# Kernel tuning notes

Measured on AMD Instinct MI355X. Metric: run time of the kernel, lower is better.

## Reference

```python
import jax, jax.numpy as jnp
import numpy as np

TAU = 1.5      # lif_tau
V_TH = 1.0     # spikingjelly default v_threshold
EPS = 1e-5     # BatchNorm eps
ALPHA = 4.0    # spikingjelly default sigmoid surrogate alpha

@jax.custom_vjp
def spike_fn(x):
    return (x >= 0.0).astype(x.dtype)

def _spike_fwd(x):
    return spike_fn(x), x

def _spike_bwd(x, g):
    s = jax.nn.sigmoid(ALPHA * x)
    return (g * ALPHA * s * (1.0 - s),)

spike_fn.defvjp(_spike_fwd, _spike_bwd)

def lif(x):
    # x: [T, B, C, N]; hard reset to 0, decay_input=True, detach_reset=True
    def step(v, xt):
        v = v + (xt - v) / TAU
        s = spike_fn(v - V_TH)
        sd = jax.lax.stop_gradient(s)
        v = (1.0 - sd) * v
        return v, s
    _, spikes = jax.lax.scan(step, jnp.zeros_like(x[0]), x)
    return spikes

def bn(x, gamma, beta, mean, var):
    # eval-mode BatchNorm1d over channel dim of [B, C, L]
    inv = gamma * jax.lax.rsqrt(var + EPS)
    return x * inv[None, :, None] + (beta - mean * inv)[None, :, None]

def setup_inputs() -> dict:
    key = jax.random.key(0)
    ks = jax.random.split(key, 13)
    B, C, T, N, H = 8, 256, 4, 4096, 1024
    return {
        "x": jax.random.normal(ks[0], (B, C, T, N), jnp.float32),
        "fc1_w": jax.random.normal(ks[1], (H, C), jnp.float32) * 0.05,
        "fc1_b": jax.random.normal(ks[2], (H,), jnp.float32) * 0.05,
        "fc2_w": jax.random.normal(ks[3], (C, H), jnp.float32) * 0.05,
        "fc2_b": jax.random.normal(ks[4], (C,), jnp.float32) * 0.05,
        "bn1_gamma": jax.random.uniform(ks[5], (H,), jnp.float32, 0.5, 1.5),
        "bn1_beta": jax.random.normal(ks[6], (H,), jnp.float32) * 0.1,
        "bn1_mean": jax.random.normal(ks[7], (H,), jnp.float32) * 0.1,
        "bn1_var": jax.random.uniform(ks[8], (H,), jnp.float32, 0.5, 1.5),
        "bn2_gamma": jax.random.uniform(ks[9], (C,), jnp.float32, 0.5, 1.5),
        "bn2_beta": jax.random.normal(ks[10], (C,), jnp.float32) * 0.1,
        "bn2_mean": jax.random.normal(ks[11], (C,), jnp.float32) * 0.1,
        "bn2_var": jax.random.uniform(ks[12], (C,), jnp.float32, 0.5, 1.5),
    }

def reference(x, fc1_w, fc1_b, fc2_w, fc2_b,
              bn1_gamma, bn1_beta, bn1_mean, bn1_var,
              bn2_gamma, bn2_beta, bn2_mean, bn2_var):
    B, C, T, N = x.shape
    H = fc1_w.shape[0]
    # fc2_bn on raw input, then LIF over T
    h = bn(x.reshape(B, C, T * N), bn2_gamma, bn2_beta, bn2_mean, bn2_var)
    h = h.reshape(B, C, T, N).transpose(2, 0, 1, 3)          # [T,B,C,N]
    h = lif(h).transpose(1, 2, 0, 3).reshape(B, C, T * N)    # [B,C,TN]
    # fc1: 1x1 conv == GEMM over channels
    h = jnp.einsum('hc,bcl->bhl', fc1_w, h) + fc1_b[None, :, None]
    h = bn(h, bn1_gamma, bn1_beta, bn1_mean, bn1_var)
    h = h.reshape(B, H, T, N).transpose(2, 0, 1, 3)          # [T,B,H,N]
    h = lif(h).transpose(1, 2, 0, 3).reshape(B, H, T * N)    # [B,H,TN]
    # fc2
    h = jnp.einsum('ch,bhl->bcl', fc2_w, h) + fc2_b[None, :, None]
    return h.reshape(B, C, T, N)
```

## Files before the change

kernel.cpp:

```cpp
#include <hip/hip_runtime.h>

#define BB 8
#define CC 256
#define TT 4
#define NNv 4096
#define HH 1024
#define LLv (TT*NNv)

typedef int int4v __attribute__((ext_vector_type(4)));

static __device__ __forceinline__ void barrier_keep_vmem() {
    asm volatile("s_waitcnt lgkmcnt(0)" ::: "memory");
    __builtin_amdgcn_s_barrier();
    __builtin_amdgcn_sched_barrier(0);
}

__global__ __launch_bounds__(256) void k_prep1(const float* __restrict__ w,
                                               unsigned char* __restrict__ wd)
{
    int i = blockIdx.x * 256 + threadIdx.x;
    int h = i >> 8, c = i & 255;
    int w24 = __float2int_rn(w[i] * 16777216.0f);
    int d2 = ((w24 + 128) & 255) - 128;  w24 = (w24 - d2) >> 8;
    int d1 = ((w24 + 128) & 255) - 128;  w24 = (w24 - d1) >> 8;
    int d0 = w24;
    size_t off = ((((size_t)(h >> 6) * 4 + (c >> 6)) * 4 + ((h >> 4) & 3)) << 10)
               + ((c >> 4) & 3) * 256 + (h & 15) * 16 + (c & 15);
    wd[off] = (unsigned char)d0;
    wd[262144 + off] = (unsigned char)d1;
    wd[2 * 262144 + off] = (unsigned char)d2;
}

__global__ __launch_bounds__(256) void k_prep2(const float* __restrict__ w,
                                               unsigned char* __restrict__ wd)
{
    int i = blockIdx.x * 256 + threadIdx.x;
    int c = i >> 10, h = i & 1023;
    int w16 = __float2int_rn(w[i] * 65536.0f);
    int d1 = ((w16 + 128) & 255) - 128;  w16 = (w16 - d1) >> 8;
    int d0 = w16;
    size_t off = ((((((size_t)(c >> 6) * 8 + (h >> 7)) * 2 + ((h >> 6) & 1)) * 4
                    + ((c >> 4) & 3)) << 10)
                 + ((h >> 4) & 3) * 256 + (c & 15) * 16 + (h & 15));
    wd[off] = (unsigned char)d0;
    wd[262144 + off] = (unsigned char)d1;
}

__global__ __launch_bounds__(256) void k_bn2_lif_t(
    const float* __restrict__ x,
    const float* __restrict__ g, const float* __restrict__ be,
    const float* __restrict__ mu, const float* __restrict__ va,
    unsigned char* __restrict__ s1T, int b0)
{
    __shared__ unsigned char ts[TT][64][80];
    int tx = threadIdx.x;
    int n0 = blockIdx.x * 64;
    int c0 = blockIdx.y * 64;
    int bl = blockIdx.z;
    int b  = b0 + bl;
    int cl = tx >> 2, np = tx & 3;
    int c = c0 + cl;
    float rsq = __fdiv_rn(1.0f, __fsqrt_rn(__fadd_rn(va[c], 1e-5f)));
    float inv = __fmul_rn(g[c], rsq);
    float add = __fsub_rn(be[c], __fmul_rn(mu[c], inv));
    size_t xb = ((size_t)(b * CC + c) * TT) * NNv + n0 + np * 16;
    float v[16];
    #pragma unroll
    for (int i = 0; i < 16; i++) v[i] = 0.0f;
    #pragma unroll
    for (int t = 0; t < TT; t++) {
        float4 p[4];
        #pragma unroll
        for (int k = 0; k < 4; k++) p[k] = *(const float4*)(x + xb + (size_t)t * NNv + 4 * k);
        const float* xp = (const float*)p;
        unsigned int ob[4] = {0, 0, 0, 0};
        #pragma unroll
        for (int i = 0; i < 16; i++) {
            float y = __fadd_rn(__fmul_rn(xp[i], inv), add);
            float vv = __fadd_rn(v[i], __fdiv_rn(__fsub_rn(y, v[i]), 1.5f));
            bool sp = vv >= 1.0f;
            v[i] = sp ? 0.0f : vv;
            if (sp) ob[i >> 2] |= 1u << (8 * (i & 3));
        }
        uint4 pk; pk.x = ob[0]; pk.y = ob[1]; pk.z = ob[2]; pk.w = ob[3];
        *(uint4*)&ts[t][cl][np * 16] = pk;
    }
    __syncthreads();
    int nl = tx >> 2, cp = tx & 3;
    #pragma unroll
    for (int t = 0; t < TT; t++) {
        unsigned int u[4];
        #pragma unroll
        for (int kk = 0; kk < 4; kk++) {
            u[kk] = (unsigned int)ts[t][cp * 16 + kk * 4 + 0][nl]
                  | ((unsigned int)ts[t][cp * 16 + kk * 4 + 1][nl] << 8)
                  | ((unsigned int)ts[t][cp * 16 + kk * 4 + 2][nl] << 16)
                  | ((unsigned int)ts[t][cp * 16 + kk * 4 + 3][nl] << 24);
        }
        uint4 pk; pk.x = u[0]; pk.y = u[1]; pk.z = u[2]; pk.w = u[3];
        *(uint4*)(s1T + ((size_t)(bl * TT + t) * NNv + n0 + nl) * CC + c0 + cp * 16) = pk;
    }
}

__global__ __launch_bounds__(256, 3) void k_gemm1_lif(
    const unsigned char* __restrict__ w1d,
    const float* __restrict__ b1,
    const float* __restrict__ g1, const float* __restrict__ be1,
    const float* __restrict__ mu1, const float* __restrict__ va1,
    const unsigned char* __restrict__ s1T, unsigned char* __restrict__ s2T)
{
    __shared__ unsigned char Ls[TT * 32][80];
    const int tx = threadIdx.x;
    const int n0 = blockIdx.x * 32;
    const int ht = blockIdx.y;
    const int bl = blockIdx.z;
    const int lane = tx & 63, w = tx >> 6;
    const int q = lane >> 4, ln = lane & 15;
    const int mh = (w & 1) * 32, wn = (w >> 1) * 16;
    const int h0 = ht * 64;

    int4v a0[TT][2], a1[TT][2], a2[TT][2];
    #pragma unroll
    for (int t = 0; t < TT; t++)
    #pragma unroll
    for (int mi = 0; mi < 2; mi++) {
        a0[t][mi] = (int4v){0, 0, 0, 0};
        a1[t][mi] = (int4v){0, 0, 0, 0};
        a2[t][mi] = (int4v){0, 0, 0, 0};
    }

    unsigned long long d[2][4];
    #pragma unroll
    for (int i = 0; i < 4; i++) {
        int task = i * 256 + tx;
        int cb = task & 7, nr = (task >> 3) & 31, t = task >> 8;
        d[0][i] = *(const unsigned long long*)(
            s1T + ((size_t)(bl * TT + t) * NNv + n0 + nr) * CC + 0 * 64 + cb * 8);
    }

    #pragma unroll
    for (int ko = 0; ko < 4; ko++) {
        const int cur = ko & 1;
        if (ko > 0) barrier_keep_vmem();
        #pragma unroll
        for (int i = 0; i < 4; i++) {
            int task = i * 256 + tx;
            int cb = task & 7, nr = (task >> 3) & 31, t = task >> 8;
            *(unsigned long long*)&Ls[t * 32 + nr][cb * 8] = d[cur][i];
        }
        if (ko < 3) {
            #pragma unroll
            for (int i = 0; i < 4; i++) {
                int task = i * 256 + tx;
                int cb = task & 7, nr = (task >> 3) & 31, t = task >> 8;
                d[cur ^ 1][i] = *(const unsigned long long*)(
                    s1T + ((size_t)(bl * TT + t) * NNv + n0 + nr) * CC + (ko + 1) * 64 + cb * 8);
            }
        }
        barrier_keep_vmem();

        int4v sf[TT];
        #pragma unroll
        for (int t = 0; t < TT; t++)
            sf[t] = *(const int4v*)&Ls[t * 32 + wn + ln][q * 16];
        int4v w0[2], w1[2], w2[2];
        #pragma unroll
        for (int mi = 0; mi < 2; mi++) {
            size_t fb = ((((size_t)ht * 4 + ko) * 4 + (mh >> 4) + mi) << 10) + lane * 16;
            w0[mi] = *(const int4v*)(w1d + fb);
            w1[mi] = *(const int4v*)(w1d + 262144 + fb);
            w2[mi] = *(const int4v*)(w1d + 2 * 262144 + fb);
        }
        #pragma unroll
        for (int t = 0; t < TT; t++)
        #pragma unroll
        for (int mi = 0; mi < 2; mi++) {
            a0[t][mi] = __builtin_amdgcn_mfma_i32_16x16x64_i8(w0[mi], sf[t], a0[t][mi], 0, 0, 0);
            a1[t][mi] = __builtin_amdgcn_mfma_i32_16x16x64_i8(w1[mi], sf[t], a1[t][mi], 0, 0, 0);
            a2[t][mi] = __builtin_amdgcn_mfma_i32_16x16x64_i8(w2[mi], sf[t], a2[t][mi], 0, 0, 0);
        }
    }

    const int l_n = n0 + wn + ln;
    #pragma unroll
    for (int mi = 0; mi < 2; mi++) {
        float invr[4], addr_[4], biasr[4];
        #pragma unroll
        for (int r = 0; r < 4; r++) {
            int h = h0 + mh + mi * 16 + q * 4 + r;
            float rsq = __fdiv_rn(1.0f, __fsqrt_rn(__fadd_rn(va1[h], 1e-5f)));
            invr[r] = __fmul_rn(g1[h], rsq);
            addr_[r] = __fsub_rn(be1[h], __fmul_rn(mu1[h], invr[r]));
            biasr[r] = b1[h];
        }
        float v4[4] = {0.f, 0.f, 0.f, 0.f};
        #pragma unroll
        for (int t = 0; t < TT; t++) {
            int4v ci = (((a0[t][mi] << 8) + a1[t][mi]) << 8) + a2[t][mi];
            unsigned int pk = 0;
            #pragma unroll
            for (int r = 0; r < 4; r++) {
                float h1 = __fadd_rn(__fmul_rn((float)ci[r], 5.9604644775390625e-08f),
                                     biasr[r]);
                float y  = __fadd_rn(__fmul_rn(h1, invr[r]), addr_[r]);
                float vv = __fadd_rn(v4[r], __fdiv_rn(__fsub_rn(y, v4[r]), 1.5f));
                bool sp = vv >= 1.0f;
                v4[r] = sp ? 0.0f : vv;
                if (sp) pk |= (1u << (8 * r));
            }
            *(unsigned int*)(s2T + ((size_t)bl * LLv + t * NNv + l_n) * HH
                             + h0 + mh + mi * 16 + q * 4) = pk;
        }
    }
}

__global__ __launch_bounds__(256, 3) void k_gemm2(
    const unsigned char* __restrict__ w2d,
    const float* __restrict__ b2c,
    const unsigned char* __restrict__ s2T, float* __restrict__ outp, int b0)
{
    __shared__ unsigned char Ls[64][144];
    const int tx = threadIdx.x;
    const int l0 = blockIdx.x * 64;
    const int ct = blockIdx.y;
    const int bl = blockIdx.z;
    const int b  = b0 + bl;
    const int lane = tx & 63, w = tx >> 6;
    const int q = lane >> 4, ln = lane & 15;
    const int mc = (w & 1) * 32, wl = (w >> 1) * 32;

    int4v a0[2][2], a1[2][2];
    #pragma unroll
    for (int mi = 0; mi < 2; mi++)
    #pragma unroll
    for (int ni = 0; ni < 2; ni++) {
        a0[mi][ni] = (int4v){0, 0, 0, 0};
        a1[mi][ni] = (int4v){0, 0, 0, 0};
    }

    unsigned long long d[2][4];
    #pragma unroll
    for (int i = 0; i < 4; i++) {
        int task = i * 256 + tx;
        int hb = task & 15, lr = task >> 4;
        d[0][i] = *(const unsigned long long*)(
            s2T + ((size_t)bl * LLv + l0 + lr) * HH + 0 * 128 + hb * 8);
    }

    #pragma unroll
    for (int ko = 0; ko < 8; ko++) {
        const int cur = ko & 1;
        if (ko > 0) barrier_keep_vmem();
        #pragma unroll
        for (int i = 0; i < 4; i++) {
            int task = i * 256 + tx;
            int hb = task & 15, lr = task >> 4;
            *(unsigned long long*)&Ls[lr][hb * 8] = d[cur][i];
        }
        if (ko < 7) {
            #pragma unroll
            for (int i = 0; i < 4; i++) {
                int task = i * 256 + tx;
                int hb = task & 15, lr = task >> 4;
                d[cur ^ 1][i] = *(const unsigned long long*)(
                    s2T + ((size_t)bl * LLv + l0 + lr) * HH + (ko + 1) * 128 + hb * 8);
            }
        }
        barrier_keep_vmem();

        #pragma unroll
        for (int kb = 0; kb < 2; kb++) {
            int4v sf[2];
            #pragma unroll
            for (int ni = 0; ni < 2; ni++)
                sf[ni] = *(const int4v*)&Ls[wl + ni * 16 + ln][kb * 64 + q * 16];
            int4v w0[2], w1[2];
            #pragma unroll
            for (int mi = 0; mi < 2; mi++) {
                size_t fb = ((((((size_t)ct * 8 + ko) * 2 + kb) * 4 + (mc >> 4) + mi)) << 10)
                          + lane * 16;
                w0[mi] = *(const int4v*)(w2d + fb);
                w1[mi] = *(const int4v*)(w2d + 262144 + fb);
            }
            #pragma unroll
            for (int mi = 0; mi < 2; mi++)
            #pragma unroll
            for (int ni = 0; ni < 2; ni++) {
                a0[mi][ni] = __builtin_amdgcn_mfma_i32_16x16x64_i8(w0[mi], sf[ni], a0[mi][ni], 0, 0, 0);
                a1[mi][ni] = __builtin_amdgcn_mfma_i32_16x16x64_i8(w1[mi], sf[ni], a1[mi][ni], 0, 0, 0);
            }
        }
    }
    #pragma unroll
    for (int mi = 0; mi < 2; mi++)
    #pragma unroll
    for (int ni = 0; ni < 2; ni++) {
        int4v tv = (a0[mi][ni] << 8) + a1[mi][ni];
        #pragma unroll
        for (int r = 0; r < 4; r++) {
            int c = ct * 64 + mc + mi * 16 + q * 4 + r;
            int l = l0 + wl + ni * 16 + ln;
            outp[((size_t)b * CC + c) * LLv + l] =
                __fadd_rn(__fmul_rn((float)tv[r], 1.52587890625e-05f), b2c[c]);
        }
    }
}

extern "C" void kernel_launch(void* const* d_in, const int* in_sizes, int n_in,
                              void* d_out, int out_size, void* d_ws, size_t ws_size,
                              hipStream_t stream) {
    const float* x    = (const float*)d_in[0];
    const float* fc1w = (const float*)d_in[1];
    const float* fc1b = (const float*)d_in[2];
    const float* fc2w = (const float*)d_in[3];
    const float* fc2b = (const float*)d_in[4];
    const float* g1   = (const float*)d_in[5];
    const float* be1  = (const float*)d_in[6];
    const float* mu1  = (const float*)d_in[7];
    const float* va1  = (const float*)d_in[8];
    const float* g2   = (const float*)d_in[9];
    const float* be2  = (const float*)d_in[10];
    const float* mu2  = (const float*)d_in[11];
    const float* va2  = (const float*)d_in[12];

    const size_t WB  = (size_t)3 * 262144 + (size_t)2 * 262144;
    const size_t S1B = (size_t)TT * NNv * CC;
    const size_t S2B = (size_t)LLv * HH;

    int nbc;
    bool full_s1;
    if      (ws_size >= WB + 8 * S1B + 8 * S2B) { nbc = 8; full_s1 = true;  }
    else if (ws_size >= WB + 8 * S1B + 4 * S2B) { nbc = 4; full_s1 = true;  }
    else if (ws_size >= WB + 8 * S1B + 2 * S2B) { nbc = 2; full_s1 = true;  }
    else if (ws_size >= WB + 8 * S1B + 1 * S2B) { nbc = 1; full_s1 = true;  }
    else                                        { nbc = 1; full_s1 = false; }

    unsigned char* w1d = (unsigned char*)d_ws;
    unsigned char* w2d = w1d + (size_t)3 * 262144;
    unsigned char* s1T = w2d + (size_t)2 * 262144;
    unsigned char* s2T = s1T + (full_s1 ? (size_t)8 * S1B : S1B);
    float* outp = (float*)d_out;

    hipLaunchKernelGGL(k_prep1, dim3(1024), dim3(256), 0, stream, fc1w, w1d);
    hipLaunchKernelGGL(k_prep2, dim3(1024), dim3(256), 0, stream, fc2w, w2d);

    if (full_s1) {
        hipLaunchKernelGGL(k_bn2_lif_t, dim3(NNv / 64, CC / 64, BB), dim3(256), 0, stream,
                           x, g2, be2, mu2, va2, s1T, 0);
        for (int b0 = 0; b0 < BB; b0 += nbc) {
            hipLaunchKernelGGL(k_gemm1_lif, dim3(NNv / 32, HH / 64, nbc), dim3(256), 0, stream,
                               w1d, fc1b, g1, be1, mu1, va1, s1T + (size_t)b0 * S1B, s2T);
            hipLaunchKernelGGL(k_gemm2, dim3(LLv / 64, CC / 64, nbc), dim3(256), 0, stream,
                               w2d, fc2b, s2T, outp, b0);
        }
    } else {
        for (int b0 = 0; b0 < BB; ++b0) {
            hipLaunchKernelGGL(k_bn2_lif_t, dim3(NNv / 64, CC / 64, 1), dim3(256), 0, stream,
                               x, g2, be2, mu2, va2, s1T, b0);
            hipLaunchKernelGGL(k_gemm1_lif, dim3(NNv / 32, HH / 64, 1), dim3(256), 0, stream,
                               w1d, fc1b, g1, be1, mu1, va1, s1T, s2T);
            hipLaunchKernelGGL(k_gemm2, dim3(LLv / 64, CC / 64, 1), dim3(256), 0, stream,
                               w2d, fc2b, s2T, outp, b0);
        }
    }
}
```

Baseline: 607.2 us.

## Stage gemm1 spike output through LDS and widen gemm2 channel tile

In the first GEMM kernel, per-lane 4-byte spike stores are now staged in shared memory and written to global memory as coalesced 16-byte rows. Weight fragment loads are issued before the barrier so their latency overlaps the wait. The second GEMM kernel now covers 128 output channels per block, with each wave taking 32 channels across all 64 columns, so each activation tile loaded into LDS is reused for twice as many channels. This halves that grid dimension and doubles the accumulator registers per thread, which may lower occupancy.

```diff
diff --git a/kernel.cpp b/kernel.cpp
--- a/kernel.cpp
+++ b/kernel.cpp
@@ -109,7 +109,7 @@
     const float* __restrict__ mu1, const float* __restrict__ va1,
     const unsigned char* __restrict__ s1T, unsigned char* __restrict__ s2T)
 {
-    __shared__ unsigned char Ls[TT * 32][80];
+    __shared__ unsigned char Lsraw[TT * 32 * 80];
     const int tx = threadIdx.x;
     const int n0 = blockIdx.x * 32;
     const int ht = blockIdx.y;
@@ -146,7 +146,7 @@
         for (int i = 0; i < 4; i++) {
             int task = i * 256 + tx;
             int cb = task & 7, nr = (task >> 3) & 31, t = task >> 8;
-            *(unsigned long long*)&Ls[t * 32 + nr][cb * 8] = d[cur][i];
+            *(unsigned long long*)(Lsraw + (t * 32 + nr) * 80 + cb * 8) = d[cur][i];
         }
         if (ko < 3) {
             #pragma unroll
@@ -157,12 +157,6 @@
                     s1T + ((size_t)(bl * TT + t) * NNv + n0 + nr) * CC + (ko + 1) * 64 + cb * 8);
             }
         }
-        barrier_keep_vmem();
-
-        int4v sf[TT];
-        #pragma unroll
-        for (int t = 0; t < TT; t++)
-            sf[t] = *(const int4v*)&Ls[t * 32 + wn + ln][q * 16];
         int4v w0[2], w1[2], w2[2];
         #pragma unroll
         for (int mi = 0; mi < 2; mi++) {
@@ -171,6 +165,12 @@
             w1[mi] = *(const int4v*)(w1d + 262144 + fb);
             w2[mi] = *(const int4v*)(w1d + 2 * 262144 + fb);
         }
+        barrier_keep_vmem();
+
+        int4v sf[TT];
+        #pragma unroll
+        for (int t = 0; t < TT; t++)
+            sf[t] = *(const int4v*)(Lsraw + (t * 32 + wn + ln) * 80 + q * 16);
         #pragma unroll
         for (int t = 0; t < TT; t++)
         #pragma unroll
@@ -181,7 +181,9 @@
         }
     }
 
-    const int l_n = n0 + wn + ln;
+    barrier_keep_vmem();
+
+    const int l_loc = wn + ln;
     #pragma unroll
     for (int mi = 0; mi < 2; mi++) {
         float invr[4], addr_[4], biasr[4];
@@ -208,9 +210,18 @@
                 v4[r] = sp ? 0.0f : vv;
                 if (sp) pk |= (1u << (8 * r));
             }
-            *(unsigned int*)(s2T + ((size_t)bl * LLv + t * NNv + l_n) * HH
-                             + h0 + mh + mi * 16 + q * 4) = pk;
-        }
+            *(unsigned int*)(Lsraw + (t * 32 + l_loc) * 80
+                             + ((mh >> 2) + mi * 4 + q) * 4) = pk;
+        }
+    }
+    __syncthreads();
+
+    #pragma unroll
+    for (int p = 0; p < 2; p++) {
+        int task = p * 256 + tx;
+        int t = task >> 7, l = (task >> 2) & 31, ch = task & 3;
+        uint4 vv = *(const uint4*)(Lsraw + (t * 32 + l) * 80 + ch * 16);
+        *(uint4*)(s2T + ((size_t)bl * LLv + t * NNv + n0 + l) * HH + h0 + ch * 16) = vv;
     }
 }
 
@@ -227,13 +238,13 @@
     const int b  = b0 + bl;
     const int lane = tx & 63, w = tx >> 6;
     const int q = lane >> 4, ln = lane & 15;
-    const int mc = (w & 1) * 32, wl = (w >> 1) * 32;
-
-    int4v a0[2][2], a1[2][2];
+    const int mc = w * 32;
+
+    int4v a0[2][4], a1[2][4];
     #pragma unroll
     for (int mi = 0; mi < 2; mi++)
     #pragma unroll
-    for (int ni = 0; ni < 2; ni++) {
+    for (int ni = 0; ni < 4; ni++) {
         a0[mi][ni] = (int4v){0, 0, 0, 0};
         a1[mi][ni] = (int4v){0, 0, 0, 0};
     }
@@ -266,40 +277,42 @@
                     s2T + ((size_t)bl * LLv + l0 + lr) * HH + (ko + 1) * 128 + hb * 8);
             }
         }
+        int4v w0[2][2], w1[2][2];
+        #pragma unroll
+        for (int kb = 0; kb < 2; kb++)
+        #pragma unroll
+        for (int mi = 0; mi < 2; mi++) {
+            size_t fb = (((((size_t)(ct * 2 + (w >> 1)) * 8 + ko) * 2 + kb) * 4
+                          + (w & 1) * 2 + mi) << 10) + lane * 16;
+            w0[kb][mi] = *(const int4v*)(w2d + fb);
+            w1[kb][mi] = *(const int4v*)(w2d + 262144 + fb);
+        }
         barrier_keep_vmem();
 
         #pragma unroll
         for (int kb = 0; kb < 2; kb++) {
-            int4v sf[2];
-            #pragma unroll
-            for (int ni = 0; ni < 2; ni++)
-                sf[ni] = *(const int4v*)&Ls[wl + ni * 16 + ln][kb * 64 + q * 16];
-            int4v w0[2], w1[2];
-            #pragma unroll
-            for (int mi = 0; mi < 2; mi++) {
-                size_t fb = ((((((size_t)ct * 8 + ko) * 2 + kb) * 4 + (mc >> 4) + mi)) << 10)
-                          + lane * 16;
-                w0[mi] = *(const int4v*)(w2d + fb);
-                w1[mi] = *(const int4v*)(w2d + 262144 + fb);
+            int4v sf[4];
+            #pragma unroll
+            for (int ni = 0; ni < 4; ni++)
+                sf[ni] = *(const int4v*)&Ls[ni * 16 + ln][kb * 64 + q * 16];
+            #pragma unroll
+            for (int mi = 0; mi < 2; mi++)
+            #pragma unroll
+            for (int ni = 0; ni < 4; ni++) {
+                a0[mi][ni] = __builtin_amdgcn_mfma_i32_16x16x64_i8(w0[kb][mi], sf[ni], a0[mi][ni], 0, 0, 0);
+                a1[mi][ni] = __builtin_amdgcn_mfma_i32_16x16x64_i8(w1[kb][mi], sf[ni], a1[mi][ni], 0, 0, 0);
             }
-            #pragma unroll
-            for (int mi = 0; mi < 2; mi++)
-            #pragma unroll
-            for (int ni = 0; ni < 2; ni++) {
-                a0[mi][ni] = __builtin_amdgcn_mfma_i32_16x16x64_i8(w0[mi], sf[ni], a0[mi][ni], 0, 0, 0);
-                a1[mi][ni] = __builtin_amdgcn_mfma_i32_16x16x64_i8(w1[mi], sf[ni], a1[mi][ni], 0, 0, 0);
-            }
         }
     }
     #pragma unroll
     for (int mi = 0; mi < 2; mi++)
     #pragma unroll
-    for (int ni = 0; ni < 2; ni++) {
+    for (int ni = 0; ni < 4; ni++) {
         int4v tv = (a0[mi][ni] << 8) + a1[mi][ni];
         #pragma unroll
         for (int r = 0; r < 4; r++) {
-            int c = ct * 64 + mc + mi * 16 + q * 4 + r;
-            int l = l0 + wl + ni * 16 + ln;
+            int c = ct * 128 + mc + mi * 16 + q * 4 + r;
+            int l = l0 + ni * 16 + ln;
             outp[((size_t)b * CC + c) * LLv + l] =
                 __fadd_rn(__fmul_rn((float)tv[r], 1.52587890625e-05f), b2c[c]);
         }
@@ -350,7 +363,7 @@
         for (int b0 = 0; b0 < BB; b0 += nbc) {
             hipLaunchKernelGGL(k_gemm1_lif, dim3(NNv / 32, HH / 64, nbc), dim3(256), 0, stream,
                                w1d, fc1b, g1, be1, mu1, va1, s1T + (size_t)b0 * S1B, s2T);
-            hipLaunchKernelGGL(k_gemm2, dim3(LLv / 64, CC / 64, nbc), dim3(256), 0, stream,
+            hipLaunchKernelGGL(k_gemm2, dim3(LLv / 64, CC / 128, nbc), dim3(256), 0, stream,
                                w2d, fc2b, s2T, outp, b0);
         }
     } else {
@@ -359,7 +372,7 @@
                                x, g2, be2, mu2, va2, s1T, b0);
             hipLaunchKernelGGL(k_gemm1_lif, dim3(NNv / 32, HH / 64, 1), dim3(256), 0, stream,
                                w1d, fc1b, g1, be1, mu1, va1, s1T, s2T);
-            hipLaunchKernelGGL(k_gemm2, dim3(LLv / 64, CC / 64, 1), dim3(256), 0, stream,
+            hipLaunchKernelGGL(k_gemm2, dim3(LLv / 64, CC / 128, 1), dim3(256), 0, stream,
                                w2d, fc2b, s2T, outp, b0);
         }
     }
```

Measured after the change: 542.9 us. -10.6%, faster.
